# Kernel optimization log

Hardware: AMD Instinct MI355X
Metric: run time of the kernel (lower is better)

Reference implementation:

```python
import jax, jax.numpy as jnp
import numpy as np

N_NODES = 100000
NEG_SLOPE = 0.01  # F.leaky_relu default


def _hetero_graphconv(x, src, dst, W, b, n_nodes):
    """HeteroGraphConv(aggregate='sum') of DGL GraphConv(norm='both') per edge type.

    x: [N, d_in]; src/dst: [R, E] int; W: [R, d_in, d_out]; b: [R, d_out].
    """
    n_rel = W.shape[0]
    ones = None
    out = jnp.zeros((n_nodes, W.shape[2]), dtype=x.dtype)
    for r in range(n_rel):  # small fixed number of relations
        s, d = src[r], dst[r]
        e_ones = jnp.ones(s.shape, dtype=x.dtype)
        deg_out = jnp.clip(jax.ops.segment_sum(e_ones, s, num_segments=n_nodes), 1.0)
        deg_in = jnp.clip(jax.ops.segment_sum(e_ones, d, num_segments=n_nodes), 1.0)
        # norm='both': scale src by out_deg^-1/2, aggregate, scale dst by in_deg^-1/2.
        # Apply weight before gather (aggregation is linear) to shrink edge traffic.
        h = (x * (deg_out ** -0.5)[:, None]) @ W[r]          # [N, d_out]
        agg = jax.ops.segment_sum(h[s], d, num_segments=n_nodes)  # gather-scatter over edges
        out = out + agg * (deg_in ** -0.5)[:, None] + b[r]
    return out


def setup_inputs() -> dict:
    key = jax.random.key(0)
    ks = jax.random.split(key, 8)
    d_in, d_h, d_out, n_cls, n_rel, n_edges = 256, 128, 128, 16, 3, 600000
    x = jax.random.normal(ks[0], (N_NODES, d_in), dtype=jnp.float32)
    src = jax.random.randint(ks[1], (n_rel, n_edges), 0, N_NODES, dtype=jnp.int32)
    dst = jax.random.randint(ks[2], (n_rel, n_edges), 0, N_NODES, dtype=jnp.int32)
    W0 = jax.random.normal(ks[3], (n_rel, d_in, d_h), dtype=jnp.float32) * (d_in ** -0.5)
    b0 = jnp.zeros((n_rel, d_h), dtype=jnp.float32)
    W1 = jax.random.normal(ks[4], (n_rel, d_h, d_out), dtype=jnp.float32) * (d_h ** -0.5)
    b1 = jnp.zeros((n_rel, d_out), dtype=jnp.float32)
    fc_W = jax.random.normal(ks[5], (d_out, n_cls), dtype=jnp.float32) * (d_out ** -0.5)
    fc_b = jnp.zeros((n_cls,), dtype=jnp.float32)
    return {"x": x, "src": src, "dst": dst, "W0": W0, "b0": b0,
            "W1": W1, "b1": b1, "fc_W": fc_W, "fc_b": fc_b}


def reference(x, src, dst, W0, b0, W1, b1, fc_W, fc_b):
    n = x.shape[0]
    h = _hetero_graphconv(x, src, dst, W0, b0, n)
    h = jax.nn.leaky_relu(h, negative_slope=NEG_SLOPE)  # dropout rate 0 (eval)
    h = _hetero_graphconv(h, src, dst, W1, b1, n)       # last layer: no activation
    logits = h @ fc_W + fc_b
    return (h, logits)
```

## Files before the change

kernel.cpp:

```cpp
#include <hip/hip_runtime.h>
#include <hip/hip_bf16.h>
#include <stdint.h>


typedef __attribute__((ext_vector_type(8))) short bf16x8;
typedef __attribute__((ext_vector_type(4))) float f32x4;
typedef unsigned short u16;

#define SCAN_T 256
#define SCAN_E 8
#define SCAN_BLK (SCAN_T * SCAN_E)
#define CUR_PAD 16
#define BF_K 8
#define HIST_K 4

__global__ __launch_bounds__(256)
void hist_kernel(const int* __restrict__ src, const int* __restrict__ dst,
                 int* __restrict__ cnt_out8, int* __restrict__ cnt_in8,
                 int E, int N) {
    int r = blockIdx.y;
    int e0 = blockIdx.x * (256 * HIST_K) + threadIdx.x;
    int copy = blockIdx.x & 7;
    size_t base = ((size_t)copy * 3 + r) * N;
    int s[HIST_K], d[HIST_K];
#pragma unroll
    for (int j = 0; j < HIST_K; j++) {
        int e = e0 + j * 256;
        bool v = e < E;
        s[j] = v ? src[(size_t)r * E + e] : -1;
        d[j] = v ? dst[(size_t)r * E + e] : -1;
    }
#pragma unroll
    for (int j = 0; j < HIST_K; j++)
        if (s[j] >= 0) atomicAdd(cnt_out8 + base + s[j], 1);
#pragma unroll
    for (int j = 0; j < HIST_K; j++)
        if (d[j] >= 0) atomicAdd(cnt_in8 + base + d[j], 1);
}

__global__ __launch_bounds__(256)
void reduce_scales_kernel(const int* __restrict__ cnt_out8, const int* __restrict__ cnt_in8,
                          float* __restrict__ s_out, float* __restrict__ s_in,
                          int* __restrict__ cnt_all, int N) {
    int n = blockIdx.x * blockDim.x + threadIdx.x;
    if (n >= N) return;
    int tot = 0;
#pragma unroll
    for (int r = 0; r < 3; r++) {
        int co = 0, ci = 0;
#pragma unroll
        for (int c = 0; c < 8; c++) {
            co += cnt_out8[((size_t)c * 3 + r) * N + n];
            ci += cnt_in8[((size_t)c * 3 + r) * N + n];
        }
        s_out[(size_t)r * N + n] = rsqrtf(fmaxf((float)co, 1.0f));
        s_in[(size_t)r * N + n]  = rsqrtf(fmaxf((float)ci, 1.0f));
        tot += ci;
    }
    cnt_all[n] = tot;
}

__global__ __launch_bounds__(SCAN_T)
void scan1_kernel(const int* __restrict__ cnt, int* __restrict__ pre,
                  int* __restrict__ bsums, int N) {
    int b = blockIdx.x, t = threadIdx.x;
    int base = b * SCAN_BLK + t * SCAN_E;
    int v[SCAN_E], s = 0;
#pragma unroll
    for (int j = 0; j < SCAN_E; j++) {
        int idx = base + j;
        v[j] = (idx < N) ? cnt[idx] : 0;
        s += v[j];
    }
    __shared__ int sd[SCAN_T];
    sd[t] = s;
    __syncthreads();
    for (int off = 1; off < SCAN_T; off <<= 1) {
        int x = (t >= off) ? sd[t - off] : 0;
        __syncthreads();
        sd[t] += x;
        __syncthreads();
    }
    if (t == SCAN_T - 1) bsums[b] = sd[t];
    int run = sd[t] - s;
#pragma unroll
    for (int j = 0; j < SCAN_E; j++) {
        int idx = base + j;
        if (idx < N) pre[idx] = run;
        run += v[j];
    }
}

__global__ void scan2_kernel(int* __restrict__ bsums, int* __restrict__ row_start,
                             int nb, int N) {
    int run = 0;
    for (int b = 0; b < nb; b++) {
        int t = bsums[b];
        bsums[b] = run;
        run += t;
    }
    row_start[N] = run;
}

__global__ __launch_bounds__(SCAN_T)
void scan3_kernel(int* __restrict__ pre, const int* __restrict__ bsums,
                  int* __restrict__ cursor, int nb, int N) {
    int b = blockIdx.x, t = threadIdx.x;
    int add = bsums[b];
    int base = b * SCAN_BLK + t * SCAN_E;
#pragma unroll
    for (int j = 0; j < SCAN_E; j++) {
        int idx = base + j;
        if (idx < N) {
            int val = pre[idx] + add;
            pre[idx] = val;
            cursor[(size_t)idx * CUR_PAD] = val;
        }
    }
}

__global__ __launch_bounds__(256)
void bucket_fill_kernel(const int* __restrict__ src, const int* __restrict__ dst,
                        int* __restrict__ cursor, int* __restrict__ esrc,
                        int E, int N) {
    int r = blockIdx.y;
    int e0 = blockIdx.x * (256 * BF_K) + threadIdx.x;
    int s[BF_K], d[BF_K], pos[BF_K];
#pragma unroll
    for (int j = 0; j < BF_K; j++) {
        int e = e0 + j * 256;
        bool v = e < E;
        s[j] = v ? src[(size_t)r * E + e] : -1;
        d[j] = v ? dst[(size_t)r * E + e] : 0;
    }
#pragma unroll
    for (int j = 0; j < BF_K; j++)
        pos[j] = (s[j] >= 0) ? atomicAdd(cursor + (size_t)d[j] * CUR_PAD, 1) : 0;
#pragma unroll
    for (int j = 0; j < BF_K; j++)
        if (s[j] >= 0) esrc[pos[j]] = r * N + s[j];
}

__global__ __launch_bounds__(256)
void prep_w_kernel(const float* __restrict__ W0, const float* __restrict__ W1,
                   u16* __restrict__ w0hi, u16* __restrict__ w0lo,
                   u16* __restrict__ w1hi, u16* __restrict__ w1lo) {
    int idx = blockIdx.x * blockDim.x + threadIdx.x;
    const int n0 = 3 * 256 * 128;
    const int n1 = 3 * 128 * 128;
    if (idx >= n0 + n1) return;
    float f;
    u16 *phi, *plo;
    int oidx;
    if (idx < n0) {
        int r = idx / 32768, rem = idx % 32768;
        int n = rem / 256, k = rem % 256;
        f = W0[(size_t)r * 32768 + (size_t)k * 128 + n];
        phi = w0hi; plo = w0lo; oidx = idx;
    } else {
        int i2 = idx - n0;
        int r = i2 / 16384, rem = i2 % 16384;
        int n = rem / 128, k = rem % 128;
        f = W1[(size_t)r * 16384 + (size_t)k * 128 + n];
        phi = w1hi; plo = w1lo; oidx = i2;
    }
    uint32_t u = __float_as_uint(f);
    phi[oidx] = (u16)(u >> 16);
    float lo = f - __uint_as_float(u & 0xFFFF0000u);
    uint32_t ul = __float_as_uint(lo);
    plo[oidx] = (u16)((ul + 0x7FFFu + ((ul >> 16) & 1u)) >> 16);
}

__global__ __launch_bounds__(256)
void gemm_split_bf16(const float* __restrict__ A, const float* __restrict__ s_out,
                     const u16* __restrict__ Whi_all, const u16* __restrict__ Wlo_all,
                     u16* __restrict__ Cout_all, int M, int K, int Nn) {
    const int r = blockIdx.y;
    const float* scale = s_out + (size_t)r * Nn;
    const u16* Whi = Whi_all + (size_t)r * K * 128;
    const u16* Wlo = Wlo_all + (size_t)r * K * 128;
    u16* Cout = Cout_all + (size_t)r * Nn * 128;

    __shared__ u16 As_hi[128][40];
    __shared__ u16 As_lo[128][40];
    __shared__ u16 Bs_hi[128][40];
    __shared__ u16 Bs_lo[128][40];

    const int tid  = threadIdx.x;
    const int m0   = blockIdx.x * 128;
    const int lane = tid & 63;
    const int wave = tid >> 6;
    const int wm   = (wave & 1) * 64;
    const int wn   = (wave >> 1) * 64;
    const int lm   = lane & 15;
    const int kq   = (lane >> 4) * 8;

    f32x4 acc[4][4];
#pragma unroll
    for (int i = 0; i < 4; i++)
#pragma unroll
        for (int j = 0; j < 4; j++) acc[i][j] = (f32x4){0.f, 0.f, 0.f, 0.f};

    const int srow = tid >> 1;
    const int skb  = (tid & 1) * 16;

    const bool valid = (m0 + srow) < M;
    const float sval = valid ? scale[m0 + srow] : 0.f;
    const float* arow = A + (size_t)(m0 + srow) * K;
    const u16* whrow = Whi + (size_t)srow * K;
    const u16* wlrow = Wlo + (size_t)srow * K;

    for (int k0 = 0; k0 < K; k0 += 32) {
        float fa[16];
        if (valid) {
            *(float4*)&fa[0]  = *(const float4*)(arow + k0 + skb);
            *(float4*)&fa[4]  = *(const float4*)(arow + k0 + skb + 4);
            *(float4*)&fa[8]  = *(const float4*)(arow + k0 + skb + 8);
            *(float4*)&fa[12] = *(const float4*)(arow + k0 + skb + 12);
        } else {
#pragma unroll
            for (int i = 0; i < 16; i++) fa[i] = 0.f;
        }
        uint32_t ah[8], al[8];
#pragma unroll
        for (int p = 0; p < 8; p++) {
            float f0 = fa[2 * p] * sval, f1 = fa[2 * p + 1] * sval;
            uint32_t u0 = __float_as_uint(f0), u1 = __float_as_uint(f1);
            ah[p] = (u0 >> 16) | (u1 & 0xFFFF0000u);
            float l0 = f0 - __uint_as_float(u0 & 0xFFFF0000u);
            float l1 = f1 - __uint_as_float(u1 & 0xFFFF0000u);
            al[p] = (__float_as_uint(l0) >> 16) | (__float_as_uint(l1) & 0xFFFF0000u);
        }
        *(uint4*)&As_hi[srow][skb]     = *(uint4*)&ah[0];
        *(uint4*)&As_hi[srow][skb + 8] = *(uint4*)&ah[4];
        *(uint4*)&As_lo[srow][skb]     = *(uint4*)&al[0];
        *(uint4*)&As_lo[srow][skb + 8] = *(uint4*)&al[4];

        *(uint4*)&Bs_hi[srow][skb]     = *(const uint4*)(whrow + k0 + skb);
        *(uint4*)&Bs_hi[srow][skb + 8] = *(const uint4*)(whrow + k0 + skb + 8);
        *(uint4*)&Bs_lo[srow][skb]     = *(const uint4*)(wlrow + k0 + skb);
        *(uint4*)&Bs_lo[srow][skb + 8] = *(const uint4*)(wlrow + k0 + skb + 8);

        __syncthreads();

        bf16x8 a_hi[4], a_lo[4], b_hi[4], b_lo[4];
#pragma unroll
        for (int i = 0; i < 4; i++) {
            a_hi[i] = *(const bf16x8*)&As_hi[wm + i * 16 + lm][kq];
            a_lo[i] = *(const bf16x8*)&As_lo[wm + i * 16 + lm][kq];
            b_hi[i] = *(const bf16x8*)&Bs_hi[wn + i * 16 + lm][kq];
            b_lo[i] = *(const bf16x8*)&Bs_lo[wn + i * 16 + lm][kq];
        }
#pragma unroll
        for (int i = 0; i < 4; i++)
#pragma unroll
            for (int j = 0; j < 4; j++) {
                acc[i][j] = __builtin_amdgcn_mfma_f32_16x16x32_bf16(a_hi[i], b_hi[j], acc[i][j], 0, 0, 0);
                acc[i][j] = __builtin_amdgcn_mfma_f32_16x16x32_bf16(a_lo[i], b_hi[j], acc[i][j], 0, 0, 0);
                acc[i][j] = __builtin_amdgcn_mfma_f32_16x16x32_bf16(a_hi[i], b_lo[j], acc[i][j], 0, 0, 0);
            }
        __syncthreads();
    }

    const int rq = (lane >> 4) * 4;
#pragma unroll
    for (int i = 0; i < 4; i++) {
        int mbase = m0 + wm + i * 16 + rq;
#pragma unroll
        for (int j = 0; j < 4; j++) {
            int col = wn + j * 16 + lm;
#pragma unroll
            for (int rg = 0; rg < 4; rg++) {
                int m = mbase + rg;
                if (m < M) {
                    uint32_t u = __float_as_uint(acc[i][j][rg]);
                    Cout[(size_t)m * 128 + col] =
                        (u16)((u + 0x7FFFu + ((u >> 16) & 1u)) >> 16);
                }
            }
        }
    }
}

#define BF16_LO(u) __uint_as_float((u) << 16)
#define BF16_HI(u) __uint_as_float((u) & 0xFFFF0000u)

__device__ __forceinline__ void gather_all(const uint32_t* __restrict__ hb32,
                                           const int* __restrict__ row_start,
                                           const int* __restrict__ esrc,
                                           const float* __restrict__ s_in,
                                           int node, int lane, int N,
                                           float& ox, float& oy) {
    const uint32_t* hrow = hb32 + lane;
    const int N2 = N * 2;
    const float w0 = s_in[node];
    const float w1 = s_in[(size_t)N + node];
    const float w2 = s_in[(size_t)N2 + node];
    const int beg = __builtin_amdgcn_readfirstlane(row_start[node]);
    const int end = __builtin_amdgcn_readfirstlane(row_start[node + 1]);
    float ax = 0.f, ay = 0.f, bx = 0.f, by = 0.f;
    float cx = 0.f, cy = 0.f, dx = 0.f, dy = 0.f;
    for (int e = beg; e < end; e += 8) {
        const int rem = end - e;
        uint32_t u[8];
        float w[8];
#pragma unroll
        for (int p = 0; p < 8; p++) {
            int idx = esrc[e + p];
            float ws = (idx < N) ? w0 : ((idx < N2) ? w1 : w2);
            bool act = p < rem;
            w[p] = act ? ws : 0.f;
            idx = act ? idx : 0;
            u[p] = hrow[(size_t)idx * 64];
        }
#pragma unroll
        for (int p = 0; p < 8; p += 4) {
            ax = fmaf(BF16_LO(u[p]),     w[p],     ax);
            ay = fmaf(BF16_HI(u[p]),     w[p],     ay);
            bx = fmaf(BF16_LO(u[p + 1]), w[p + 1], bx);
            by = fmaf(BF16_HI(u[p + 1]), w[p + 1], by);
            cx = fmaf(BF16_LO(u[p + 2]), w[p + 2], cx);
            cy = fmaf(BF16_HI(u[p + 2]), w[p + 2], cy);
            dx = fmaf(BF16_LO(u[p + 3]), w[p + 3], dx);
            dy = fmaf(BF16_HI(u[p + 3]), w[p + 3], dy);
        }
    }
    ox = (ax + bx) + (cx + dx);
    oy = (ay + by) + (cy + dy);
}

__global__ __launch_bounds__(256)
void gather_l0(const u16* __restrict__ hb, const int* __restrict__ row_start,
               const int* __restrict__ esrc, const float* __restrict__ s_in,
               const float* __restrict__ b, float* __restrict__ out, int N) {
    int node = blockIdx.x * 4 + (threadIdx.x >> 6);
    if (node >= N) return;
    int lane = threadIdx.x & 63;
    float tx, ty;
    gather_all((const uint32_t*)hb, row_start, esrc, s_in, node, lane, N, tx, ty);
    int c0 = lane * 2;
    tx += b[c0] + b[128 + c0] + b[256 + c0];
    ty += b[c0 + 1] + b[128 + c0 + 1] + b[256 + c0 + 1];
    tx = fmaxf(tx, 0.f) + 0.01f * fminf(tx, 0.f);
    ty = fmaxf(ty, 0.f) + 0.01f * fminf(ty, 0.f);
    *(float2*)(out + (size_t)node * 128 + c0) = make_float2(tx, ty);
}

__global__ __launch_bounds__(256)
void gather_l1(const u16* __restrict__ hb, const int* __restrict__ row_start,
               const int* __restrict__ esrc, const float* __restrict__ s_in,
               const float* __restrict__ b, const float* __restrict__ fcW,
               const float* __restrict__ fcb, float* __restrict__ out_h,
               float* __restrict__ out_logits, int N) {
    int node = blockIdx.x * 4 + (threadIdx.x >> 6);
    if (node >= N) return;
    int lane = threadIdx.x & 63;
    float tx, ty;
    gather_all((const uint32_t*)hb, row_start, esrc, s_in, node, lane, N, tx, ty);
    int c0 = lane * 2;
    tx += b[c0] + b[128 + c0] + b[256 + c0];
    ty += b[c0 + 1] + b[128 + c0 + 1] + b[256 + c0 + 1];
    *(float2*)(out_h + (size_t)node * 128 + c0) = make_float2(tx, ty);

    const float* fc0 = fcW + (size_t)c0 * 16;
    float p[16];
#pragma unroll
    for (int j = 0; j < 16; j++) p[j] = tx * fc0[j] + ty * fc0[16 + j];
#pragma unroll
    for (int off = 1; off < 64; off <<= 1) {
#pragma unroll
        for (int j = 0; j < 16; j++) p[j] += __shfl_xor(p[j], off);
    }
    if (lane == 0) {
        float* lp = out_logits + (size_t)node * 16;
        *(float4*)(lp + 0)  = make_float4(p[0] + fcb[0],  p[1] + fcb[1],  p[2] + fcb[2],  p[3] + fcb[3]);
        *(float4*)(lp + 4)  = make_float4(p[4] + fcb[4],  p[5] + fcb[5],  p[6] + fcb[6],  p[7] + fcb[7]);
        *(float4*)(lp + 8)  = make_float4(p[8] + fcb[8],  p[9] + fcb[9],  p[10] + fcb[10], p[11] + fcb[11]);
        *(float4*)(lp + 12) = make_float4(p[12] + fcb[12], p[13] + fcb[13], p[14] + fcb[14], p[15] + fcb[15]);
    }
}

extern "C" void kernel_launch(void* const* d_in, const int* in_sizes, int n_in,
                              void* d_out, int out_size, void* d_ws, size_t ws_size,
                              hipStream_t stream) {
    const float* x   = (const float*)d_in[0];
    const int*   src = (const int*)d_in[1];
    const int*   dst = (const int*)d_in[2];
    const float* W0  = (const float*)d_in[3];
    const float* b0  = (const float*)d_in[4];
    const float* W1  = (const float*)d_in[5];
    const float* b1  = (const float*)d_in[6];
    const float* fcW = (const float*)d_in[7];
    const float* fcb = (const float*)d_in[8];

    const int N = in_sizes[0] / 256;
    const int E = in_sizes[1] / 3;
    const int nb = (N + SCAN_BLK - 1) / SCAN_BLK;

    float* out_h      = (float*)d_out;
    float* out_logits = out_h + (size_t)N * 128;

    char* p = (char*)d_ws;
    auto alloc = [&](size_t bytes) -> char* {
        char* q = p;
        p += (bytes + 255) & ~(size_t)255;
        return q;
    };
    float* s_out     = (float*)alloc(3 * (size_t)N * 4);
    float* s_in      = (float*)alloc(3 * (size_t)N * 4);
    int*   cnt8      = (int*)alloc(2 * 8 * 3 * (size_t)N * 4);
    int*   cnt_out8  = cnt8;
    int*   cnt_in8   = cnt8 + 8 * 3 * (size_t)N;
    int*   cnt_all   = (int*)alloc((size_t)N * 4);
    int*   row_start = (int*)alloc((size_t)(N + 1) * 4);
    int*   cursor    = (int*)alloc((size_t)N * CUR_PAD * 4);
    int*   bsums     = (int*)alloc(1024 * 4);
    int*   esrc      = (int*)alloc(3 * (size_t)E * 4 + 256);
    u16*   w0hi      = (u16*)alloc(3 * 256 * 128 * 2);
    u16*   w0lo      = (u16*)alloc(3 * 256 * 128 * 2);
    u16*   w1hi      = (u16*)alloc(3 * 128 * 128 * 2);
    u16*   w1lo      = (u16*)alloc(3 * 128 * 128 * 2);
    u16*   hb        = (u16*)alloc(3 * (size_t)N * 128 * 2);
    float* acc0      = (float*)alloc((size_t)N * 128 * 4);

    hipMemsetAsync(cnt8, 0, 2 * 8 * 3 * (size_t)N * sizeof(int), stream);

    hist_kernel<<<dim3((E + 256 * HIST_K - 1) / (256 * HIST_K), 3), 256, 0, stream>>>(
        src, dst, cnt_out8, cnt_in8, E, N);
    reduce_scales_kernel<<<(N + 255) / 256, 256, 0, stream>>>(
        cnt_out8, cnt_in8, s_out, s_in, cnt_all, N);

    scan1_kernel<<<nb, SCAN_T, 0, stream>>>(cnt_all, row_start, bsums, N);
    scan2_kernel<<<1, 1, 0, stream>>>(bsums, row_start, nb, N);
    scan3_kernel<<<nb, SCAN_T, 0, stream>>>(row_start, bsums, cursor, nb, N);
    bucket_fill_kernel<<<dim3((E + 256 * BF_K - 1) / (256 * BF_K), 3), 256, 0, stream>>>(
        src, dst, cursor, esrc, E, N);

    prep_w_kernel<<<(3 * 256 * 128 + 3 * 128 * 128 + 255) / 256, 256, 0, stream>>>(
        W0, W1, w0hi, w0lo, w1hi, w1lo);

    int gemm_blocks   = (N + 127) / 128;
    int gather_blocks = (N + 3) / 4;

    gemm_split_bf16<<<dim3(gemm_blocks, 3), 256, 0, stream>>>(
        x, s_out, w0hi, w0lo, hb, N, 256, N);
    gather_l0<<<gather_blocks, 256, 0, stream>>>(hb, row_start, esrc, s_in, b0, acc0, N);

    gemm_split_bf16<<<dim3(gemm_blocks, 3), 256, 0, stream>>>(
        acc0, s_out, w1hi, w1lo, hb, N, 128, N);
    gather_l1<<<gather_blocks, 256, 0, stream>>>(hb, row_start, esrc, s_in, b1, fcW, fcb,
                                                 out_h, out_logits, N);
}
```

Before: 758.5 us.

## Gather two destination nodes per wavefront with 8-byte loads and deeper unroll

```diff
diff --git a/kernel.cpp b/kernel.cpp
--- a/kernel.cpp
+++ b/kernel.cpp
@@ -13,6 +13,7 @@
 #define CUR_PAD 16
 #define BF_K 8
 #define HIST_K 4
+#define NSLOT 12
 
 __global__ __launch_bounds__(256)
 void hist_kernel(const int* __restrict__ src, const int* __restrict__ dst,
@@ -285,65 +286,84 @@
 #define BF16_LO(u) __uint_as_float((u) << 16)
 #define BF16_HI(u) __uint_as_float((u) & 0xFFFF0000u)
 
-__device__ __forceinline__ void gather_all(const uint32_t* __restrict__ hb32,
-                                           const int* __restrict__ row_start,
-                                           const int* __restrict__ esrc,
-                                           const float* __restrict__ s_in,
-                                           int node, int lane, int N,
-                                           float& ox, float& oy) {
-    const uint32_t* hrow = hb32 + lane;
+__device__ __forceinline__ void gather_pair(const uint32_t* __restrict__ hb32,
+                                            const int* __restrict__ row_start,
+                                            const int* __restrict__ esrc,
+                                            const float* __restrict__ s_in,
+                                            int snodeA, int nodeBr, int half,
+                                            int lane31, int N, float acc[4]) {
     const int N2 = N * 2;
-    const float w0 = s_in[node];
-    const float w1 = s_in[(size_t)N + node];
-    const float w2 = s_in[(size_t)N2 + node];
-    const int beg = __builtin_amdgcn_readfirstlane(row_start[node]);
-    const int end = __builtin_amdgcn_readfirstlane(row_start[node + 1]);
-    float ax = 0.f, ay = 0.f, bx = 0.f, by = 0.f;
-    float cx = 0.f, cy = 0.f, dx = 0.f, dy = 0.f;
-    for (int e = beg; e < end; e += 8) {
-        const int rem = end - e;
-        uint32_t u[8];
-        float w[8];
-#pragma unroll
-        for (int p = 0; p < 8; p++) {
-            int idx = esrc[e + p];
+    const int snodeB = (nodeBr < N) ? nodeBr : (N - 1);
+    const int begA = __builtin_amdgcn_readfirstlane(row_start[snodeA]);
+    const int endA = __builtin_amdgcn_readfirstlane(row_start[snodeA + 1]);
+    const int begB = __builtin_amdgcn_readfirstlane(row_start[snodeB]);
+    const int endB = __builtin_amdgcn_readfirstlane(row_start[snodeB + 1]);
+    const int degA = endA - begA, degB = endB - begB;
+    const int maxdeg = degA > degB ? degA : degB;
+
+    float wA0 = s_in[snodeA], wA1 = s_in[(size_t)N + snodeA], wA2 = s_in[(size_t)N2 + snodeA];
+    float wB0 = s_in[snodeB], wB1 = s_in[(size_t)N + snodeB], wB2 = s_in[(size_t)N2 + snodeB];
+    if (nodeBr >= N) { wB0 = 0.f; wB1 = 0.f; wB2 = 0.f; }
+
+    const float w0 = half ? wB0 : wA0;
+    const float w1 = half ? wB1 : wA1;
+    const float w2 = half ? wB2 : wA2;
+    const int   deg = half ? degB : degA;
+    const uint32_t* hcol = hb32 + lane31 * 2;
+
+    for (int j = 0; j < maxdeg; j += NSLOT) {
+        uint2 u[NSLOT];
+        float w[NSLOT];
+#pragma unroll
+        for (int p = 0; p < NSLOT; p++) {
+            int iA = esrc[begA + j + p];
+            int iB = esrc[begB + j + p];
+            int idx = half ? iB : iA;
             float ws = (idx < N) ? w0 : ((idx < N2) ? w1 : w2);
-            bool act = p < rem;
+            bool act = (j + p) < deg;
             w[p] = act ? ws : 0.f;
             idx = act ? idx : 0;
-            u[p] = hrow[(size_t)idx * 64];
-        }
-#pragma unroll
-        for (int p = 0; p < 8; p += 4) {
-            ax = fmaf(BF16_LO(u[p]),     w[p],     ax);
-            ay = fmaf(BF16_HI(u[p]),     w[p],     ay);
-            bx = fmaf(BF16_LO(u[p + 1]), w[p + 1], bx);
-            by = fmaf(BF16_HI(u[p + 1]), w[p + 1], by);
-            cx = fmaf(BF16_LO(u[p + 2]), w[p + 2], cx);
-            cy = fmaf(BF16_HI(u[p + 2]), w[p + 2], cy);
-            dx = fmaf(BF16_LO(u[p + 3]), w[p + 3], dx);
-            dy = fmaf(BF16_HI(u[p + 3]), w[p + 3], dy);
-        }
-    }
-    ox = (ax + bx) + (cx + dx);
-    oy = (ay + by) + (cy + dy);
+            u[p] = *(const uint2*)(hcol + (size_t)idx * 64);
+        }
+#pragma unroll
+        for (int p = 0; p < NSLOT; p++) {
+            acc[0] = fmaf(BF16_LO(u[p].x), w[p], acc[0]);
+            acc[1] = fmaf(BF16_HI(u[p].x), w[p], acc[1]);
+            acc[2] = fmaf(BF16_LO(u[p].y), w[p], acc[2]);
+            acc[3] = fmaf(BF16_HI(u[p].y), w[p], acc[3]);
+        }
+    }
 }
 
 __global__ __launch_bounds__(256)
 void gather_l0(const u16* __restrict__ hb, const int* __restrict__ row_start,
                const int* __restrict__ esrc, const float* __restrict__ s_in,
                const float* __restrict__ b, float* __restrict__ out, int N) {
-    int node = blockIdx.x * 4 + (threadIdx.x >> 6);
-    if (node >= N) return;
-    int lane = threadIdx.x & 63;
-    float tx, ty;
-    gather_all((const uint32_t*)hb, row_start, esrc, s_in, node, lane, N, tx, ty);
-    int c0 = lane * 2;
-    tx += b[c0] + b[128 + c0] + b[256 + c0];
-    ty += b[c0 + 1] + b[128 + c0 + 1] + b[256 + c0 + 1];
-    tx = fmaxf(tx, 0.f) + 0.01f * fminf(tx, 0.f);
-    ty = fmaxf(ty, 0.f) + 0.01f * fminf(ty, 0.f);
-    *(float2*)(out + (size_t)node * 128 + c0) = make_float2(tx, ty);
+    int wv = threadIdx.x >> 6;
+    int t = threadIdx.x & 63;
+    int half = t >> 5;
+    int lane31 = t & 31;
+    int snodeA = __builtin_amdgcn_readfirstlane(blockIdx.x * 8 + wv * 2);
+    if (snodeA >= N) return;
+    int nodeBr = snodeA + 1;
+    float acc[4] = {0.f, 0.f, 0.f, 0.f};
+    gather_pair((const uint32_t*)hb, row_start, esrc, s_in,
+                snodeA, nodeBr, half, lane31, N, acc);
+    int node = half ? nodeBr : snodeA;
+    int c0 = lane31 * 4;
+    float4 b0v = *(const float4*)(b + c0);
+    float4 b1v = *(const float4*)(b + 128 + c0);
+    float4 b2v = *(const float4*)(b + 256 + c0);
+    float bs[4] = {b0v.x + b1v.x + b2v.x, b0v.y + b1v.y + b2v.y,
+                   b0v.z + b1v.z + b2v.z, b0v.w + b1v.w + b2v.w};
+    float4 o;
+    float* po = (float*)&o;
+#pragma unroll
+    for (int k = 0; k < 4; k++) {
+        float v = acc[k] + bs[k];
+        po[k] = fmaxf(v, 0.f) + 0.01f * fminf(v, 0.f);
+    }
+    if (node < N) *(float4*)(out + (size_t)node * 128 + c0) = o;
 }
 
 __global__ __launch_bounds__(256)
@@ -352,26 +372,42 @@
                const float* __restrict__ b, const float* __restrict__ fcW,
                const float* __restrict__ fcb, float* __restrict__ out_h,
                float* __restrict__ out_logits, int N) {
-    int node = blockIdx.x * 4 + (threadIdx.x >> 6);
-    if (node >= N) return;
-    int lane = threadIdx.x & 63;
-    float tx, ty;
-    gather_all((const uint32_t*)hb, row_start, esrc, s_in, node, lane, N, tx, ty);
-    int c0 = lane * 2;
-    tx += b[c0] + b[128 + c0] + b[256 + c0];
-    ty += b[c0 + 1] + b[128 + c0 + 1] + b[256 + c0 + 1];
-    *(float2*)(out_h + (size_t)node * 128 + c0) = make_float2(tx, ty);
-
-    const float* fc0 = fcW + (size_t)c0 * 16;
+    int wv = threadIdx.x >> 6;
+    int t = threadIdx.x & 63;
+    int half = t >> 5;
+    int lane31 = t & 31;
+    int snodeA = __builtin_amdgcn_readfirstlane(blockIdx.x * 8 + wv * 2);
+    if (snodeA >= N) return;
+    int nodeBr = snodeA + 1;
+    float acc[4] = {0.f, 0.f, 0.f, 0.f};
+    gather_pair((const uint32_t*)hb, row_start, esrc, s_in,
+                snodeA, nodeBr, half, lane31, N, acc);
+    int node = half ? nodeBr : snodeA;
+    int c0 = lane31 * 4;
+    float4 b0v = *(const float4*)(b + c0);
+    float4 b1v = *(const float4*)(b + 128 + c0);
+    float4 b2v = *(const float4*)(b + 256 + c0);
+    float v[4] = {acc[0] + b0v.x + b1v.x + b2v.x, acc[1] + b0v.y + b1v.y + b2v.y,
+                  acc[2] + b0v.z + b1v.z + b2v.z, acc[3] + b0v.w + b1v.w + b2v.w};
+    if (node < N) {
+        float4 o = make_float4(v[0], v[1], v[2], v[3]);
+        *(float4*)(out_h + (size_t)node * 128 + c0) = o;
+    }
+
     float p[16];
 #pragma unroll
-    for (int j = 0; j < 16; j++) p[j] = tx * fc0[j] + ty * fc0[16 + j];
-#pragma unroll
-    for (int off = 1; off < 64; off <<= 1) {
-#pragma unroll
-        for (int j = 0; j < 16; j++) p[j] += __shfl_xor(p[j], off);
-    }
-    if (lane == 0) {
+    for (int jj = 0; jj < 16; jj++) {
+        p[jj] = v[0] * fcW[(size_t)(c0 + 0) * 16 + jj]
+              + v[1] * fcW[(size_t)(c0 + 1) * 16 + jj]
+              + v[2] * fcW[(size_t)(c0 + 2) * 16 + jj]
+              + v[3] * fcW[(size_t)(c0 + 3) * 16 + jj];
+    }
+#pragma unroll
+    for (int off = 1; off <= 16; off <<= 1) {
+#pragma unroll
+        for (int jj = 0; jj < 16; jj++) p[jj] += __shfl_xor(p[jj], off);
+    }
+    if (lane31 == 0 && node < N) {
         float* lp = out_logits + (size_t)node * 16;
         *(float4*)(lp + 0)  = make_float4(p[0] + fcb[0],  p[1] + fcb[1],  p[2] + fcb[2],  p[3] + fcb[3]);
         *(float4*)(lp + 4)  = make_float4(p[4] + fcb[4],  p[5] + fcb[5],  p[6] + fcb[6],  p[7] + fcb[7]);
@@ -415,7 +451,7 @@
     int*   row_start = (int*)alloc((size_t)(N + 1) * 4);
     int*   cursor    = (int*)alloc((size_t)N * CUR_PAD * 4);
     int*   bsums     = (int*)alloc(1024 * 4);
-    int*   esrc      = (int*)alloc(3 * (size_t)E * 4 + 256);
+    int*   esrc      = (int*)alloc(3 * (size_t)E * 4 + 1024);
     u16*   w0hi      = (u16*)alloc(3 * 256 * 128 * 2);
     u16*   w0lo      = (u16*)alloc(3 * 256 * 128 * 2);
     u16*   w1hi      = (u16*)alloc(3 * 128 * 128 * 2);
@@ -440,7 +476,7 @@
         W0, W1, w0hi, w0lo, w1hi, w1lo);
 
     int gemm_blocks   = (N + 127) / 128;
-    int gather_blocks = (N + 3) / 4;
+    int gather_blocks = (N + 7) / 8;
 
     gemm_split_bf16<<<dim3(gemm_blocks, 3), 256, 0, stream>>>(
         x, s_out, w0hi, w0lo, hb, N, 256, N);
```

Measured after the change: 768.1 us. Within noise of the previous version (+1.3%).

## Split GNN layers into per-relation GEMM and gather passes with separate CSR

Applied to the files above, without the earlier changes.

```diff
diff --git a/kernel.cpp b/kernel.cpp
--- a/kernel.cpp
+++ b/kernel.cpp
@@ -41,10 +41,9 @@
 __global__ __launch_bounds__(256)
 void reduce_scales_kernel(const int* __restrict__ cnt_out8, const int* __restrict__ cnt_in8,
                           float* __restrict__ s_out, float* __restrict__ s_in,
-                          int* __restrict__ cnt_all, int N) {
+                          int* __restrict__ cnt_in, int N) {
     int n = blockIdx.x * blockDim.x + threadIdx.x;
     if (n >= N) return;
-    int tot = 0;
 #pragma unroll
     for (int r = 0; r < 3; r++) {
         int co = 0, ci = 0;
@@ -55,21 +54,20 @@
         }
         s_out[(size_t)r * N + n] = rsqrtf(fmaxf((float)co, 1.0f));
         s_in[(size_t)r * N + n]  = rsqrtf(fmaxf((float)ci, 1.0f));
-        tot += ci;
-    }
-    cnt_all[n] = tot;
+        cnt_in[(size_t)r * N + n] = ci;
+    }
 }
 
 __global__ __launch_bounds__(SCAN_T)
 void scan1_kernel(const int* __restrict__ cnt, int* __restrict__ pre,
                   int* __restrict__ bsums, int N) {
-    int b = blockIdx.x, t = threadIdx.x;
+    int r = blockIdx.y, b = blockIdx.x, t = threadIdx.x;
     int base = b * SCAN_BLK + t * SCAN_E;
     int v[SCAN_E], s = 0;
 #pragma unroll
     for (int j = 0; j < SCAN_E; j++) {
         int idx = base + j;
-        v[j] = (idx < N) ? cnt[idx] : 0;
+        v[j] = (idx < N) ? cnt[(size_t)r * N + idx] : 0;
         s += v[j];
     }
     __shared__ int sd[SCAN_T];
@@ -81,40 +79,42 @@
         sd[t] += x;
         __syncthreads();
     }
-    if (t == SCAN_T - 1) bsums[b] = sd[t];
+    if (t == SCAN_T - 1) bsums[r * gridDim.x + b] = sd[t];
     int run = sd[t] - s;
 #pragma unroll
     for (int j = 0; j < SCAN_E; j++) {
         int idx = base + j;
-        if (idx < N) pre[idx] = run;
+        if (idx < N) pre[(size_t)r * (N + 1) + idx] = run;
         run += v[j];
     }
 }
 
 __global__ void scan2_kernel(int* __restrict__ bsums, int* __restrict__ row_start,
                              int nb, int N) {
-    int run = 0;
-    for (int b = 0; b < nb; b++) {
-        int t = bsums[b];
-        bsums[b] = run;
-        run += t;
-    }
-    row_start[N] = run;
+    for (int r = 0; r < 3; r++) {
+        int run = 0;
+        for (int b = 0; b < nb; b++) {
+            int t = bsums[r * nb + b];
+            bsums[r * nb + b] = run;
+            run += t;
+        }
+        row_start[(size_t)r * (N + 1) + N] = run;
+    }
 }
 
 __global__ __launch_bounds__(SCAN_T)
 void scan3_kernel(int* __restrict__ pre, const int* __restrict__ bsums,
                   int* __restrict__ cursor, int nb, int N) {
-    int b = blockIdx.x, t = threadIdx.x;
-    int add = bsums[b];
+    int r = blockIdx.y, b = blockIdx.x, t = threadIdx.x;
+    int add = bsums[r * nb + b];
     int base = b * SCAN_BLK + t * SCAN_E;
 #pragma unroll
     for (int j = 0; j < SCAN_E; j++) {
         int idx = base + j;
         if (idx < N) {
-            int val = pre[idx] + add;
-            pre[idx] = val;
-            cursor[(size_t)idx * CUR_PAD] = val;
+            int val = pre[(size_t)r * (N + 1) + idx] + add;
+            pre[(size_t)r * (N + 1) + idx] = val;
+            cursor[((size_t)r * N + idx) * CUR_PAD] = val;
         }
     }
 }
@@ -122,7 +122,7 @@
 __global__ __launch_bounds__(256)
 void bucket_fill_kernel(const int* __restrict__ src, const int* __restrict__ dst,
                         int* __restrict__ cursor, int* __restrict__ esrc,
-                        int E, int N) {
+                        int E, int EP, int N) {
     int r = blockIdx.y;
     int e0 = blockIdx.x * (256 * BF_K) + threadIdx.x;
     int s[BF_K], d[BF_K], pos[BF_K];
@@ -135,10 +135,10 @@
     }
 #pragma unroll
     for (int j = 0; j < BF_K; j++)
-        pos[j] = (s[j] >= 0) ? atomicAdd(cursor + (size_t)d[j] * CUR_PAD, 1) : 0;
+        pos[j] = (s[j] >= 0) ? atomicAdd(cursor + ((size_t)r * N + d[j]) * CUR_PAD, 1) : 0;
 #pragma unroll
     for (int j = 0; j < BF_K; j++)
-        if (s[j] >= 0) esrc[pos[j]] = r * N + s[j];
+        if (s[j] >= 0) esrc[(size_t)r * EP + pos[j]] = s[j];
 }
 
 __global__ __launch_bounds__(256)
@@ -172,15 +172,9 @@
 }
 
 __global__ __launch_bounds__(256)
-void gemm_split_bf16(const float* __restrict__ A, const float* __restrict__ s_out,
-                     const u16* __restrict__ Whi_all, const u16* __restrict__ Wlo_all,
-                     u16* __restrict__ Cout_all, int M, int K, int Nn) {
-    const int r = blockIdx.y;
-    const float* scale = s_out + (size_t)r * Nn;
-    const u16* Whi = Whi_all + (size_t)r * K * 128;
-    const u16* Wlo = Wlo_all + (size_t)r * K * 128;
-    u16* Cout = Cout_all + (size_t)r * Nn * 128;
-
+void gemm_split_bf16(const float* __restrict__ A, const float* __restrict__ scale,
+                     const u16* __restrict__ Whi, const u16* __restrict__ Wlo,
+                     u16* __restrict__ Cout, int M, int K) {
     __shared__ u16 As_hi[128][40];
     __shared__ u16 As_lo[128][40];
     __shared__ u16 Bs_hi[128][40];
@@ -285,82 +279,97 @@
 #define BF16_LO(u) __uint_as_float((u) << 16)
 #define BF16_HI(u) __uint_as_float((u) & 0xFFFF0000u)
 
-__device__ __forceinline__ void gather_all(const uint32_t* __restrict__ hb32,
-                                           const int* __restrict__ row_start,
-                                           const int* __restrict__ esrc,
-                                           const float* __restrict__ s_in,
-                                           int node, int lane, int N,
-                                           float& ox, float& oy) {
+__device__ __forceinline__ void gather_rel_sum(const uint32_t* __restrict__ hb32,
+                                               const int* __restrict__ rs,
+                                               const int* __restrict__ es,
+                                               int node, int lane, int N,
+                                               float& sx, float& sy) {
     const uint32_t* hrow = hb32 + lane;
-    const int N2 = N * 2;
-    const float w0 = s_in[node];
-    const float w1 = s_in[(size_t)N + node];
-    const float w2 = s_in[(size_t)N2 + node];
-    const int beg = __builtin_amdgcn_readfirstlane(row_start[node]);
-    const int end = __builtin_amdgcn_readfirstlane(row_start[node + 1]);
+    const int beg = __builtin_amdgcn_readfirstlane(rs[node]);
+    const int end = __builtin_amdgcn_readfirstlane(rs[node + 1]);
     float ax = 0.f, ay = 0.f, bx = 0.f, by = 0.f;
     float cx = 0.f, cy = 0.f, dx = 0.f, dy = 0.f;
     for (int e = beg; e < end; e += 8) {
         const int rem = end - e;
         uint32_t u[8];
-        float w[8];
 #pragma unroll
         for (int p = 0; p < 8; p++) {
-            int idx = esrc[e + p];
-            float ws = (idx < N) ? w0 : ((idx < N2) ? w1 : w2);
-            bool act = p < rem;
-            w[p] = act ? ws : 0.f;
-            idx = act ? idx : 0;
+            int iv = es[e + p];
+            int idx = (p < rem) ? iv : N;
             u[p] = hrow[(size_t)idx * 64];
         }
-#pragma unroll
-        for (int p = 0; p < 8; p += 4) {
-            ax = fmaf(BF16_LO(u[p]),     w[p],     ax);
-            ay = fmaf(BF16_HI(u[p]),     w[p],     ay);
-            bx = fmaf(BF16_LO(u[p + 1]), w[p + 1], bx);
-            by = fmaf(BF16_HI(u[p + 1]), w[p + 1], by);
-            cx = fmaf(BF16_LO(u[p + 2]), w[p + 2], cx);
-            cy = fmaf(BF16_HI(u[p + 2]), w[p + 2], cy);
-            dx = fmaf(BF16_LO(u[p + 3]), w[p + 3], dx);
-            dy = fmaf(BF16_HI(u[p + 3]), w[p + 3], dy);
-        }
-    }
-    ox = (ax + bx) + (cx + dx);
-    oy = (ay + by) + (cy + dy);
-}
-
-__global__ __launch_bounds__(256)
-void gather_l0(const u16* __restrict__ hb, const int* __restrict__ row_start,
-               const int* __restrict__ esrc, const float* __restrict__ s_in,
-               const float* __restrict__ b, float* __restrict__ out, int N) {
+        ax += BF16_LO(u[0]); ay += BF16_HI(u[0]);
+        bx += BF16_LO(u[1]); by += BF16_HI(u[1]);
+        cx += BF16_LO(u[2]); cy += BF16_HI(u[2]);
+        dx += BF16_LO(u[3]); dy += BF16_HI(u[3]);
+        ax += BF16_LO(u[4]); ay += BF16_HI(u[4]);
+        bx += BF16_LO(u[5]); by += BF16_HI(u[5]);
+        cx += BF16_LO(u[6]); cy += BF16_HI(u[6]);
+        dx += BF16_LO(u[7]); dy += BF16_HI(u[7]);
+    }
+    sx = (ax + bx) + (cx + dx);
+    sy = (ay + by) + (cy + dy);
+}
+
+__global__ __launch_bounds__(256)
+void gather_pass(const u16* __restrict__ hb_r, const int* __restrict__ rs,
+                 const int* __restrict__ es, const float* __restrict__ w_all,
+                 float* __restrict__ accbuf, int N, int init) {
     int node = blockIdx.x * 4 + (threadIdx.x >> 6);
     if (node >= N) return;
     int lane = threadIdx.x & 63;
-    float tx, ty;
-    gather_all((const uint32_t*)hb, row_start, esrc, s_in, node, lane, N, tx, ty);
+    float sx, sy;
+    gather_rel_sum((const uint32_t*)hb_r, rs, es, node, lane, N, sx, sy);
+    float w = w_all[node];
+    float tx = sx * w, ty = sy * w;
+    float2* ap = (float2*)(accbuf + (size_t)node * 128 + lane * 2);
+    if (init) {
+        *ap = make_float2(tx, ty);
+    } else {
+        float2 a = *ap;
+        *ap = make_float2(a.x + tx, a.y + ty);
+    }
+}
+
+__global__ __launch_bounds__(256)
+void gather_fin0(const u16* __restrict__ hb_r, const int* __restrict__ rs,
+                 const int* __restrict__ es, const float* __restrict__ w_all,
+                 const float* __restrict__ accbuf, const float* __restrict__ b,
+                 float* __restrict__ out, int N) {
+    int node = blockIdx.x * 4 + (threadIdx.x >> 6);
+    if (node >= N) return;
+    int lane = threadIdx.x & 63;
+    float sx, sy;
+    gather_rel_sum((const uint32_t*)hb_r, rs, es, node, lane, N, sx, sy);
+    float w = w_all[node];
+    float2 a = *(const float2*)(accbuf + (size_t)node * 128 + lane * 2);
     int c0 = lane * 2;
-    tx += b[c0] + b[128 + c0] + b[256 + c0];
-    ty += b[c0 + 1] + b[128 + c0 + 1] + b[256 + c0 + 1];
+    float tx = sx * w + a.x + b[c0] + b[128 + c0] + b[256 + c0];
+    float ty = sy * w + a.y + b[c0 + 1] + b[128 + c0 + 1] + b[256 + c0 + 1];
     tx = fmaxf(tx, 0.f) + 0.01f * fminf(tx, 0.f);
     ty = fmaxf(ty, 0.f) + 0.01f * fminf(ty, 0.f);
     *(float2*)(out + (size_t)node * 128 + c0) = make_float2(tx, ty);
 }
 
 __global__ __launch_bounds__(256)
-void gather_l1(const u16* __restrict__ hb, const int* __restrict__ row_start,
-               const int* __restrict__ esrc, const float* __restrict__ s_in,
-               const float* __restrict__ b, const float* __restrict__ fcW,
-               const float* __restrict__ fcb, float* __restrict__ out_h,
-               float* __restrict__ out_logits, int N) {
+void gather_fin1(const u16* __restrict__ hb_r, const int* __restrict__ rs,
+                 const int* __restrict__ es, const float* __restrict__ w_all,
+                 const float* __restrict__ accbuf, const float* __restrict__ b,
+                 const float* __restrict__ fcW, const float* __restrict__ fcb,
+                 float* __restrict__ out_h, float* __restrict__ out_logits, int N) {
     int node = blockIdx.x * 4 + (threadIdx.x >> 6);
     if (node >= N) return;
     int lane = threadIdx.x & 63;
-    float tx, ty;
-    gather_all((const uint32_t*)hb, row_start, esrc, s_in, node, lane, N, tx, ty);
+    float sx, sy;
+    gather_rel_sum((const uint32_t*)hb_r, rs, es, node, lane, N, sx, sy);
+    float w = w_all[node];
+    float2 a = *(const float2*)(accbuf + (size_t)node * 128 + lane * 2);
     int c0 = lane * 2;
-    tx += b[c0] + b[128 + c0] + b[256 + c0];
-    ty += b[c0 + 1] + b[128 + c0 + 1] + b[256 + c0 + 1];
-    *(float2*)(out_h + (size_t)node * 128 + c0) = make_float2(tx, ty);
+    float tx = sx * w + a.x + b[c0] + b[128 + c0] + b[256 + c0];
+    float ty = sy * w + a.y + b[c0 + 1] + b[128 + c0 + 1] + b[256 + c0 + 1];
+    typedef __attribute__((ext_vector_type(2))) float f32x2;
+    f32x2 oh = {tx, ty};
+    __builtin_nontemporal_store(oh, (f32x2*)(out_h + (size_t)node * 128 + c0));
 
     const float* fc0 = fcW + (size_t)c0 * 16;
     float p[16];
@@ -373,10 +382,14 @@
     }
     if (lane == 0) {
         float* lp = out_logits + (size_t)node * 16;
-        *(float4*)(lp + 0)  = make_float4(p[0] + fcb[0],  p[1] + fcb[1],  p[2] + fcb[2],  p[3] + fcb[3]);
-        *(float4*)(lp + 4)  = make_float4(p[4] + fcb[4],  p[5] + fcb[5],  p[6] + fcb[6],  p[7] + fcb[7]);
-        *(float4*)(lp + 8)  = make_float4(p[8] + fcb[8],  p[9] + fcb[9],  p[10] + fcb[10], p[11] + fcb[11]);
-        *(float4*)(lp + 12) = make_float4(p[12] + fcb[12], p[13] + fcb[13], p[14] + fcb[14], p[15] + fcb[15]);
+        f32x4 q0 = {p[0] + fcb[0],  p[1] + fcb[1],  p[2] + fcb[2],  p[3] + fcb[3]};
+        f32x4 q1 = {p[4] + fcb[4],  p[5] + fcb[5],  p[6] + fcb[6],  p[7] + fcb[7]};
+        f32x4 q2 = {p[8] + fcb[8],  p[9] + fcb[9],  p[10] + fcb[10], p[11] + fcb[11]};
+        f32x4 q3 = {p[12] + fcb[12], p[13] + fcb[13], p[14] + fcb[14], p[15] + fcb[15]};
+        __builtin_nontemporal_store(q0, (f32x4*)(lp + 0));
+        __builtin_nontemporal_store(q1, (f32x4*)(lp + 4));
+        __builtin_nontemporal_store(q2, (f32x4*)(lp + 8));
+        __builtin_nontemporal_store(q3, (f32x4*)(lp + 12));
     }
 }
 
@@ -395,7 +408,9 @@
 
     const int N = in_sizes[0] / 256;
     const int E = in_sizes[1] / 3;
+    const int EP = E + 64;
     const int nb = (N + SCAN_BLK - 1) / SCAN_BLK;
+    const size_t HBR = (size_t)(N + 1) * 128;
 
     float* out_h      = (float*)d_out;
     float* out_logits = out_h + (size_t)N * 128;
@@ -411,30 +426,33 @@
     int*   cnt8      = (int*)alloc(2 * 8 * 3 * (size_t)N * 4);
     int*   cnt_out8  = cnt8;
     int*   cnt_in8   = cnt8 + 8 * 3 * (size_t)N;
-    int*   cnt_all   = (int*)alloc((size_t)N * 4);
-    int*   row_start = (int*)alloc((size_t)(N + 1) * 4);
-    int*   cursor    = (int*)alloc((size_t)N * CUR_PAD * 4);
+    int*   cnt_in    = (int*)alloc(3 * (size_t)N * 4);
+    int*   row_start = (int*)alloc(3 * (size_t)(N + 1) * 4);
+    int*   cursor    = (int*)alloc(3 * (size_t)N * CUR_PAD * 4);
     int*   bsums     = (int*)alloc(1024 * 4);
-    int*   esrc      = (int*)alloc(3 * (size_t)E * 4 + 256);
+    int*   esrc      = (int*)alloc(3 * (size_t)EP * 4);
     u16*   w0hi      = (u16*)alloc(3 * 256 * 128 * 2);
     u16*   w0lo      = (u16*)alloc(3 * 256 * 128 * 2);
     u16*   w1hi      = (u16*)alloc(3 * 128 * 128 * 2);
     u16*   w1lo      = (u16*)alloc(3 * 128 * 128 * 2);
-    u16*   hb        = (u16*)alloc(3 * (size_t)N * 128 * 2);
+    u16*   hb        = (u16*)alloc(3 * HBR * 2);
     float* acc0      = (float*)alloc((size_t)N * 128 * 4);
+    float* accbuf    = (float*)alloc((size_t)N * 128 * 4);
 
     hipMemsetAsync(cnt8, 0, 2 * 8 * 3 * (size_t)N * sizeof(int), stream);
+    for (int r = 0; r < 3; r++)
+        hipMemsetAsync(hb + r * HBR + (size_t)N * 128, 0, 128 * 2, stream);
 
     hist_kernel<<<dim3((E + 256 * HIST_K - 1) / (256 * HIST_K), 3), 256, 0, stream>>>(
         src, dst, cnt_out8, cnt_in8, E, N);
     reduce_scales_kernel<<<(N + 255) / 256, 256, 0, stream>>>(
-        cnt_out8, cnt_in8, s_out, s_in, cnt_all, N);
-
-    scan1_kernel<<<nb, SCAN_T, 0, stream>>>(cnt_all, row_start, bsums, N);
+        cnt_out8, cnt_in8, s_out, s_in, cnt_in, N);
+
+    scan1_kernel<<<dim3(nb, 3), SCAN_T, 0, stream>>>(cnt_in, row_start, bsums, N);
     scan2_kernel<<<1, 1, 0, stream>>>(bsums, row_start, nb, N);
-    scan3_kernel<<<nb, SCAN_T, 0, stream>>>(row_start, bsums, cursor, nb, N);
+    scan3_kernel<<<dim3(nb, 3), SCAN_T, 0, stream>>>(row_start, bsums, cursor, nb, N);
     bucket_fill_kernel<<<dim3((E + 256 * BF_K - 1) / (256 * BF_K), 3), 256, 0, stream>>>(
-        src, dst, cursor, esrc, E, N);
+        src, dst, cursor, esrc, E, EP, N);
 
     prep_w_kernel<<<(3 * 256 * 128 + 3 * 128 * 128 + 255) / 256, 256, 0, stream>>>(
         W0, W1, w0hi, w0lo, w1hi, w1lo);
@@ -442,12 +460,32 @@
     int gemm_blocks   = (N + 127) / 128;
     int gather_blocks = (N + 3) / 4;
 
-    gemm_split_bf16<<<dim3(gemm_blocks, 3), 256, 0, stream>>>(
-        x, s_out, w0hi, w0lo, hb, N, 256, N);
-    gather_l0<<<gather_blocks, 256, 0, stream>>>(hb, row_start, esrc, s_in, b0, acc0, N);
-
-    gemm_split_bf16<<<dim3(gemm_blocks, 3), 256, 0, stream>>>(
-        acc0, s_out, w1hi, w1lo, hb, N, 128, N);
-    gather_l1<<<gather_blocks, 256, 0, stream>>>(hb, row_start, esrc, s_in, b1, fcW, fcb,
-                                                 out_h, out_logits, N);
-}
+    for (int r = 0; r < 3; r++) {
+        gemm_split_bf16<<<gemm_blocks, 256, 0, stream>>>(
+            x, s_out + (size_t)r * N, w0hi + (size_t)r * 256 * 128,
+            w0lo + (size_t)r * 256 * 128, hb + r * HBR, N, 256);
+        const u16* hbr = hb + r * HBR;
+        const int* rs  = row_start + (size_t)r * (N + 1);
+        const int* es  = esrc + (size_t)r * EP;
+        const float* w = s_in + (size_t)r * N;
+        if (r < 2)
+            gather_pass<<<gather_blocks, 256, 0, stream>>>(hbr, rs, es, w, accbuf, N, r == 0);
+        else
+            gather_fin0<<<gather_blocks, 256, 0, stream>>>(hbr, rs, es, w, accbuf, b0, acc0, N);
+    }
+
+    for (int r = 0; r < 3; r++) {
+        gemm_split_bf16<<<gemm_blocks, 256, 0, stream>>>(
+            acc0, s_out + (size_t)r * N, w1hi + (size_t)r * 128 * 128,
+            w1lo + (size_t)r * 128 * 128, hb + r * HBR, N, 128);
+        const u16* hbr = hb + r * HBR;
+        const int* rs  = row_start + (size_t)r * (N + 1);
+        const int* es  = esrc + (size_t)r * EP;
+        const float* w = s_in + (size_t)r * N;
+        if (r < 2)
+            gather_pass<<<gather_blocks, 256, 0, stream>>>(hbr, rs, es, w, accbuf, N, r == 0);
+        else
+            gather_fin1<<<gather_blocks, 256, 0, stream>>>(hbr, rs, es, w, accbuf, b1,
+                                                           fcW, fcb, out_h, out_logits, N);
+    }
+}
```

After: 939.5 us. 23.9% more time.
